# Optimization experiments

Measured on AMD Instinct MI355X. Metric: run time of the kernel, lower is better.

The kernel has to match this reference:

```python
import jax, jax.numpy as jnp
import numpy as np

S, B, K = 64, 16, 512
QD, KD, A = 512, 512, 256


def setup_inputs() -> dict:
    key = jax.random.key(0)
    ks = jax.random.split(key, 10)
    inv_q = 1.0 / np.sqrt(QD)
    inv_k = 1.0 / np.sqrt(KD)
    inv_a = 1.0 / np.sqrt(A)
    return {
        "queries": jax.random.normal(ks[0], (S, B, QD), dtype=jnp.float32),
        "keys": jax.random.normal(ks[1], (B, K, KD), dtype=jnp.float32),
        "null_mask": jax.random.randint(ks[2], (B, K), 0, 2).astype(jnp.bool_),
        # nn.Linear params (PyTorch layout: weight (out, in), bias (out,))
        "Ww": jax.random.uniform(ks[3], (A, QD), jnp.float32, -inv_q, inv_q),
        "Wb": jax.random.uniform(ks[4], (A,), jnp.float32, -inv_q, inv_q),
        "Uw": jax.random.uniform(ks[5], (A, KD), jnp.float32, -inv_k, inv_k),
        "Ub": jax.random.uniform(ks[6], (A,), jnp.float32, -inv_k, inv_k),
        "vw": jax.random.uniform(ks[7], (1, A), jnp.float32, -inv_a, inv_a),
        "vb": jax.random.uniform(ks[8], (1,), jnp.float32, -inv_a, inv_a),
    }


def reference(queries, keys, null_mask, Ww, Wb, Uw, Ub, vw, vb):
    # t_query: (S, B, A); t_key: (B, K, A)
    t_query = jnp.einsum("sbq,aq->sba", queries, Ww) + Wb
    t_key = jnp.einsum("bkd,ad->bka", keys, Uw) + Ub
    # broadcast add -> (S, B, K, A), tanh, project with v -> alpha (S, B, K)
    h = jnp.tanh(t_query[:, :, None, :] + t_key[None, :, :, :])
    alpha = jnp.einsum("sbka,a->sbk", h, vw[0]) + vb[0]
    alpha = jnp.where(null_mask[None, :, :], -jnp.inf, alpha)
    att_weight = jax.nn.softmax(alpha, axis=2)  # (S, B, K)
    # bmm(att_weight^T, keys)^T -> (S, B, KD)
    attened_keys = jnp.einsum("sbk,bkd->sbd", att_weight, keys)
    return attened_keys, alpha
```

## Files before the change

### kernel.cpp

```cpp
#include <hip/hip_runtime.h>
#include <math.h>

#define S_DIM 64
#define B_DIM 16
#define K_DIM 512
#define QD_DIM 512
#define A_DIM 256

#define NEG_BIG (-3.0e38f)

#define SC 2.8853900817779268f

#define EKBF_BYTE_OFF 1048576
#define W_WS_BYTE_OFF 5242880
#define CONV_BYTE_OFF 7340032
#define CONV_ROWS 9728

typedef __attribute__((ext_vector_type(8))) short short8v;
typedef __attribute__((ext_vector_type(4))) float f32x4;

static __device__ __forceinline__ uint2 pack_hi4(float4 v) {
    unsigned x0 = __float_as_uint(v.x), x1 = __float_as_uint(v.y),
             x2 = __float_as_uint(v.z), x3 = __float_as_uint(v.w);
    uint2 r;
    r.x = (x1 & 0xffff0000u) | (x0 >> 16);
    r.y = (x3 & 0xffff0000u) | (x2 >> 16);
    return r;
}
static __device__ __forceinline__ uint2 pack_lo4(float4 v) {
    float l0 = v.x - __uint_as_float(__float_as_uint(v.x) & 0xffff0000u);
    float l1 = v.y - __uint_as_float(__float_as_uint(v.y) & 0xffff0000u);
    float l2 = v.z - __uint_as_float(__float_as_uint(v.z) & 0xffff0000u);
    float l3 = v.w - __uint_as_float(__float_as_uint(v.w) & 0xffff0000u);
    unsigned y0 = __float_as_uint(l0), y1 = __float_as_uint(l1),
             y2 = __float_as_uint(l2), y3 = __float_as_uint(l3);
    uint2 r;
    r.x = (y1 & 0xffff0000u) | (y0 >> 16);
    r.y = (y3 & 0xffff0000u) | (y2 >> 16);
    return r;
}

static __device__ __forceinline__ unsigned short bf16_rne(float f) {
    unsigned u = __float_as_uint(f);
    return (unsigned short)((u + 0x7FFFu + ((u >> 16) & 1u)) >> 16);
}

__global__ __launch_bounds__(256) void conv_kernel(
    const float* __restrict__ q, const float* __restrict__ k,
    const float* __restrict__ ww, const float* __restrict__ uw,
    unsigned short* __restrict__ hi, unsigned short* __restrict__ lo)
{
    const int idx = blockIdx.x * 256 + threadIdx.x;
    const int row = idx >> 6;
    const int c   = (idx & 63) << 3;

    const float* __restrict__ src;
    if (row < 1024)      src = q  + (size_t)row * 512;
    else if (row < 9216) src = k  + (size_t)(row - 1024) * 512;
    else if (row < 9472) src = ww + (size_t)(row - 9216) * 512;
    else                 src = uw + (size_t)(row - 9472) * 512;

    float4 v0 = *(const float4*)(src + c);
    float4 v1 = *(const float4*)(src + c + 4);
    uint2 h0 = pack_hi4(v0), h1 = pack_hi4(v1);
    uint2 l0 = pack_lo4(v0), l1 = pack_lo4(v1);
    uint4 H = {h0.x, h0.y, h1.x, h1.y};
    uint4 L = {l0.x, l0.y, l1.x, l1.y};
    *(uint4*)&hi[(size_t)row * 512 + c] = H;
    *(uint4*)&lo[(size_t)row * 512 + c] = L;
}

__global__ __launch_bounds__(256) void lin_mfma(
    const unsigned short* __restrict__ hi, const unsigned short* __restrict__ lo,
    const float* __restrict__ Wb, const float* __restrict__ Ub,
    float* __restrict__ eq, unsigned short* __restrict__ ekbf)
{
    __shared__ unsigned short Ah[64][40], Al[64][40], Bh[64][40], Bl[64][40];

    const int bx = blockIdx.x;
    const bool isQ = (bx < 64);
    int mt, nt;
    if (isQ) { mt = bx >> 2; nt = bx & 3; }
    else     { int t = bx - 64; mt = t >> 7; nt = t & 127; }

    const int aro = isQ ? (mt * 64) : (9472 + mt * 64);
    const int bro = isQ ? (9216 + nt * 64) : (1024 + nt * 64);

    const int tid  = threadIdx.x;
    const int srow = tid >> 2;
    const int scol = (tid & 3) << 3;
    const int lane = tid & 63, wid = tid >> 6;
    const int wm = (wid >> 1) << 5, wn = (wid & 1) << 5;
    const int fr  = lane & 15;
    const int fkb = (lane >> 4) << 3;

    f32x4 acc[2][2] = {};

    const unsigned short* pAh = hi + (size_t)(aro + srow) * 512 + scol;
    const unsigned short* pAl = lo + (size_t)(aro + srow) * 512 + scol;
    const unsigned short* pBh = hi + (size_t)(bro + srow) * 512 + scol;
    const unsigned short* pBl = lo + (size_t)(bro + srow) * 512 + scol;

    uint4 c_ah = *(const uint4*)(pAh);
    uint4 c_al = *(const uint4*)(pAl);
    uint4 c_bh = *(const uint4*)(pBh);
    uint4 c_bl = *(const uint4*)(pBl);
    uint4 n_ah = *(const uint4*)(pAh + 32);
    uint4 n_al = *(const uint4*)(pAl + 32);
    uint4 n_bh = *(const uint4*)(pBh + 32);
    uint4 n_bl = *(const uint4*)(pBl + 32);

    for (int ks = 0; ks < 16; ++ks) {
        __syncthreads();
        *(uint4*)&Ah[srow][scol] = c_ah;
        *(uint4*)&Al[srow][scol] = c_al;
        *(uint4*)&Bh[srow][scol] = c_bh;
        *(uint4*)&Bl[srow][scol] = c_bl;
        __syncthreads();
        c_ah = n_ah; c_al = n_al; c_bh = n_bh; c_bl = n_bl;
        if (ks < 14) {
            const int o = (ks + 2) * 32;
            n_ah = *(const uint4*)(pAh + o);
            n_al = *(const uint4*)(pAl + o);
            n_bh = *(const uint4*)(pBh + o);
            n_bl = *(const uint4*)(pBl + o);
        }
        short8v bhv[2], blv[2];
        #pragma unroll
        for (int j = 0; j < 2; ++j) {
            bhv[j] = *(const short8v*)&Bh[wn + j * 16 + fr][fkb];
            blv[j] = *(const short8v*)&Bl[wn + j * 16 + fr][fkb];
        }
        #pragma unroll
        for (int i = 0; i < 2; ++i) {
            short8v ah = *(const short8v*)&Ah[wm + i * 16 + fr][fkb];
            short8v al = *(const short8v*)&Al[wm + i * 16 + fr][fkb];
            #pragma unroll
            for (int j = 0; j < 2; ++j) {
                acc[i][j] = __builtin_amdgcn_mfma_f32_16x16x32_bf16(ah, bhv[j], acc[i][j], 0, 0, 0);
                acc[i][j] = __builtin_amdgcn_mfma_f32_16x16x32_bf16(ah, blv[j], acc[i][j], 0, 0, 0);
                acc[i][j] = __builtin_amdgcn_mfma_f32_16x16x32_bf16(al, bhv[j], acc[i][j], 0, 0, 0);
            }
        }
    }

    const int crow = (lane >> 4) << 2;
    if (isQ) {
        #pragma unroll
        for (int j = 0; j < 2; ++j) {
            const int a_col = nt * 64 + wn + j * 16 + fr;
            const float bias = Wb[a_col];
            #pragma unroll
            for (int i = 0; i < 2; ++i)
                #pragma unroll
                for (int r = 0; r < 4; ++r) {
                    const int m = mt * 64 + wm + i * 16 + crow + r;
                    eq[(size_t)m * 256 + a_col] =
                        __builtin_amdgcn_exp2f(SC * (acc[i][j][r] + bias));
                }
        }
    } else {
        #pragma unroll
        for (int i = 0; i < 2; ++i)
            #pragma unroll
            for (int r = 0; r < 4; ++r) {
                const int a = mt * 64 + wm + i * 16 + crow + r;
                const float bias = Ub[a];
                #pragma unroll
                for (int j = 0; j < 2; ++j) {
                    const int n = nt * 64 + wn + j * 16 + fr;
                    float e = __builtin_amdgcn_exp2f(SC * (acc[i][j][r] + bias));
                    ekbf[(size_t)(n >> 9) * 131072 + (size_t)a * 512 + (n & 511)]
                        = bf16_rne(e);
                }
            }
    }
}

__global__ __launch_bounds__(256) void alpha_kernel(
    const float* __restrict__ eq, const unsigned short* __restrict__ ekbf,
    const float* __restrict__ vw, const float* __restrict__ vb,
    const unsigned char* __restrict__ mask,
    float* __restrict__ alpha_out, float* __restrict__ w_ws)
{
    __shared__ float4 pv4[128];
    __shared__ float red[3][4];

    const int bid = blockIdx.x;
    const int b = bid >> 6;
    const int s = bid & 63;
    const int sb = s * B_DIM + b;
    const int tid = threadIdx.x;
    const int lane = tid & 63, wid = tid >> 6;

    const float myvw = vw[tid];
    if (tid < 128) {
        float2 e2 = *(const float2*)&eq[(size_t)sb * A_DIM + tid * 2];
        float2 v2 = *(const float2*)&vw[tid * 2];
        float4 p = {e2.x, e2.y, v2.x, v2.y};
        pv4[tid] = p;
    }

    float sv = myvw;
    #pragma unroll
    for (int o = 32; o > 0; o >>= 1) sv += __shfl_xor(sv, o);
    if (lane == 0) red[0][wid] = sv;
    __syncthreads();
    const float base = red[0][0] + red[0][1] + red[0][2] + red[0][3] + vb[0];

    const unsigned short* __restrict__ ekb = ekbf + (size_t)b * 131072;
    const int k2 = tid * 2;

    float acc0 = 0.f, acc1 = 0.f;
    #pragma unroll 4
    for (int ap = 0; ap < 128; ++ap) {
        unsigned va = *(const unsigned*)&ekb[(size_t)(2 * ap) * 512 + k2];
        unsigned vbu = *(const unsigned*)&ekb[(size_t)(2 * ap + 1) * 512 + k2];
        float4 p = pv4[ap];
        float e0a = __uint_as_float(va << 16);
        float e1a = __uint_as_float(va & 0xffff0000u);
        float e0b = __uint_as_float(vbu << 16);
        float e1b = __uint_as_float(vbu & 0xffff0000u);
        float d00 = fmaf(p.x, e0a, 1.0f);
        float d01 = fmaf(p.y, e0b, 1.0f);
        float d10 = fmaf(p.x, e1a, 1.0f);
        float d11 = fmaf(p.y, e1b, 1.0f);
        float n0 = fmaf(p.w, d00, p.z * d01);
        float n1 = fmaf(p.w, d10, p.z * d11);
        float r0 = __builtin_amdgcn_rcpf(d00 * d01);
        float r1 = __builtin_amdgcn_rcpf(d10 * d11);
        acc0 = fmaf(n0, r0, acc0);
        acc1 = fmaf(n1, r1, acc1);
    }

    float a0 = base - 2.0f * acc0;
    float a1 = base - 2.0f * acc1;
    const unsigned char* mrow = mask + b * K_DIM;
    if (mrow[k2])     a0 = NEG_BIG;
    if (mrow[k2 + 1]) a1 = NEG_BIG;

    *(float2*)&alpha_out[(size_t)sb * K_DIM + k2] = make_float2(a0, a1);

    float m = fmaxf(a0, a1);
    #pragma unroll
    for (int o = 32; o > 0; o >>= 1) m = fmaxf(m, __shfl_xor(m, o));
    if (lane == 0) red[1][wid] = m;
    __syncthreads();
    const float mx = fmaxf(fmaxf(red[1][0], red[1][1]), fmaxf(red[1][2], red[1][3]));

    float e0 = __expf(a0 - mx);
    float e1 = __expf(a1 - mx);
    float ssum = e0 + e1;
    #pragma unroll
    for (int o = 32; o > 0; o >>= 1) ssum += __shfl_xor(ssum, o);
    if (lane == 0) red[2][wid] = ssum;
    __syncthreads();
    const float inv = 1.0f / (red[2][0] + red[2][1] + red[2][2] + red[2][3]);

    *(float2*)&w_ws[(size_t)(b * S_DIM + s) * K_DIM + k2] = make_float2(e0 * inv, e1 * inv);
}

__global__ __launch_bounds__(256) void att_kernel(
    const float* __restrict__ w_ws, const float* __restrict__ keys,
    float* __restrict__ out_att)
{
    __shared__ float wt[16][68];
    __shared__ float kt[64][64];

    const int d0g = blockIdx.x * 64;
    const int s0  = blockIdx.y * 16;
    const int b   = blockIdx.z;
    const int tid = threadIdx.x;

    const int sL = tid >> 4;
    const int dc = (tid & 15) << 2;

    float acc[4] = {};

    for (int k0 = 0; k0 < K_DIM; k0 += 64) {
        __syncthreads();
        *(float4*)&wt[sL][dc] =
            *(const float4*)&w_ws[(size_t)(b * S_DIM + s0 + sL) * K_DIM + k0 + dc];
        #pragma unroll
        for (int rr = 0; rr < 4; ++rr) {
            const int kr = (tid >> 4) + rr * 16;
            *(float4*)&kt[kr][dc] =
                *(const float4*)&keys[((size_t)b * K_DIM + k0 + kr) * QD_DIM + d0g + dc];
        }
        __syncthreads();
        #pragma unroll
        for (int kk = 0; kk < 64; kk += 4) {
            float4 wv = *(const float4*)&wt[sL][kk];
            float wr[4] = {wv.x, wv.y, wv.z, wv.w};
            #pragma unroll
            for (int u = 0; u < 4; ++u) {
                float4 kv = *(const float4*)&kt[kk + u][dc];
                acc[0] = fmaf(wr[u], kv.x, acc[0]);
                acc[1] = fmaf(wr[u], kv.y, acc[1]);
                acc[2] = fmaf(wr[u], kv.z, acc[2]);
                acc[3] = fmaf(wr[u], kv.w, acc[3]);
            }
        }
    }

    float4 o = {acc[0], acc[1], acc[2], acc[3]};
    *(float4*)&out_att[(size_t)((s0 + sL) * B_DIM + b) * QD_DIM + d0g + dc] = o;
}

extern "C" void kernel_launch(void* const* d_in, const int* in_sizes, int n_in,
                              void* d_out, int out_size, void* d_ws, size_t ws_size,
                              hipStream_t stream) {
    const float* queries = (const float*)d_in[0];
    const float* keys    = (const float*)d_in[1];
    const unsigned char* mask = (const unsigned char*)d_in[2];
    const float* Ww = (const float*)d_in[3];
    const float* Wb = (const float*)d_in[4];
    const float* Uw = (const float*)d_in[5];
    const float* Ub = (const float*)d_in[6];
    const float* vw = (const float*)d_in[7];
    const float* vb = (const float*)d_in[8];

    float* out_att   = (float*)d_out;
    float* out_alpha = (float*)d_out + (size_t)S_DIM * B_DIM * QD_DIM;

    char* ws = (char*)d_ws;
    float* eq            = (float*)ws;
    unsigned short* ekbf = (unsigned short*)(ws + EKBF_BYTE_OFF);
    float* w_ws          = (float*)(ws + W_WS_BYTE_OFF);
    unsigned short* hi   = (unsigned short*)(ws + CONV_BYTE_OFF);
    unsigned short* lo   = hi + (size_t)CONV_ROWS * 512;

    conv_kernel<<<2432, 256, 0, stream>>>(queries, keys, Ww, Uw, hi, lo);

    lin_mfma<<<576, 256, 0, stream>>>(hi, lo, Wb, Ub, eq, ekbf);

    alpha_kernel<<<1024, 256, 0, stream>>>(eq, ekbf, vw, vb, mask,
                                           out_alpha, w_ws);

    dim3 gC(QD_DIM / 64, S_DIM / 16, B_DIM);
    att_kernel<<<gC, 256, 0, stream>>>(w_ws, keys, out_att);
    att_kernel<<<gC, 256, 0, stream>>>(w_ws, keys, out_att);
    att_kernel<<<gC, 256, 0, stream>>>(w_ws, keys, out_att);
}
```

Baseline: 166.4 us.

## Compute attention-weighted keys with bf16 MFMA and drop redundant launches

Softmax weights are now written as packed bf16 instead of fp32. The attention-weighted sum over keys is rewritten as a bf16 MFMA GEMM, with the fp32 keys converted to bf16 fragments in shared memory. The grid changes to one block per 64 output columns per batch, covering all 64 queries. The previous triple launch of the attention kernel becomes a single launch. The aim is to cut the FMA-bound scalar work and halve weight traffic, at the cost of bf16 precision on the weights and keys.

```diff
diff --git a/kernel.cpp b/kernel.cpp
--- a/kernel.cpp
+++ b/kernel.cpp
@@ -181,7 +181,7 @@
     const float* __restrict__ eq, const unsigned short* __restrict__ ekbf,
     const float* __restrict__ vw, const float* __restrict__ vb,
     const unsigned char* __restrict__ mask,
-    float* __restrict__ alpha_out, float* __restrict__ w_ws)
+    float* __restrict__ alpha_out, unsigned short* __restrict__ w_bf)
 {
     __shared__ float4 pv4[128];
     __shared__ float red[3][4];
@@ -257,54 +257,76 @@
     __syncthreads();
     const float inv = 1.0f / (red[2][0] + red[2][1] + red[2][2] + red[2][3]);
 
-    *(float2*)&w_ws[(size_t)(b * S_DIM + s) * K_DIM + k2] = make_float2(e0 * inv, e1 * inv);
-}
-
-__global__ __launch_bounds__(256) void att_kernel(
-    const float* __restrict__ w_ws, const float* __restrict__ keys,
+    const unsigned wpack = (unsigned)bf16_rne(e0 * inv)
+                         | ((unsigned)bf16_rne(e1 * inv) << 16);
+    *(unsigned*)&w_bf[(size_t)(b * S_DIM + s) * K_DIM + k2] = wpack;
+}
+
+__global__ __launch_bounds__(256) void att_mfma(
+    const unsigned short* __restrict__ w_bf, const float* __restrict__ keys,
     float* __restrict__ out_att)
 {
-    __shared__ float wt[16][68];
-    __shared__ float kt[64][64];
-
-    const int d0g = blockIdx.x * 64;
-    const int s0  = blockIdx.y * 16;
-    const int b   = blockIdx.z;
+    __shared__ unsigned short Wt[64][40];
+    __shared__ float Ks[32][68];
+
+    const int n0 = blockIdx.x * 64;
+    const int b  = blockIdx.y;
     const int tid = threadIdx.x;
-
-    const int sL = tid >> 4;
-    const int dc = (tid & 15) << 2;
-
-    float acc[4] = {};
-
-    for (int k0 = 0; k0 < K_DIM; k0 += 64) {
+    const int lane = tid & 63, wid = tid >> 6;
+    const int wm = (wid >> 1) << 5, wn = (wid & 1) << 5;
+    const int fr  = lane & 15;
+    const int fkb = (lane >> 4) << 3;
+
+    const int ws_row = tid >> 2;
+    const int ws_c8  = (tid & 3) << 3;
+    const int ks_row = tid >> 3;
+    const int ks_c8  = (tid & 7) << 3;
+
+    f32x4 acc[2][2] = {};
+
+    for (int k0 = 0; k0 < K_DIM; k0 += 32) {
         __syncthreads();
-        *(float4*)&wt[sL][dc] =
-            *(const float4*)&w_ws[(size_t)(b * S_DIM + s0 + sL) * K_DIM + k0 + dc];
-        #pragma unroll
-        for (int rr = 0; rr < 4; ++rr) {
-            const int kr = (tid >> 4) + rr * 16;
-            *(float4*)&kt[kr][dc] =
-                *(const float4*)&keys[((size_t)b * K_DIM + k0 + kr) * QD_DIM + d0g + dc];
+        *(uint4*)&Wt[ws_row][ws_c8] =
+            *(const uint4*)&w_bf[(size_t)(b * S_DIM + ws_row) * K_DIM + k0 + ws_c8];
+        {
+            const float* src = keys + ((size_t)b * K_DIM + k0 + ks_row) * QD_DIM + n0 + ks_c8;
+            *(float4*)&Ks[ks_row][ks_c8]     = *(const float4*)src;
+            *(float4*)&Ks[ks_row][ks_c8 + 4] = *(const float4*)(src + 4);
         }
         __syncthreads();
-        #pragma unroll
-        for (int kk = 0; kk < 64; kk += 4) {
-            float4 wv = *(const float4*)&wt[sL][kk];
-            float wr[4] = {wv.x, wv.y, wv.z, wv.w};
-            #pragma unroll
-            for (int u = 0; u < 4; ++u) {
-                float4 kv = *(const float4*)&kt[kk + u][dc];
-                acc[0] = fmaf(wr[u], kv.x, acc[0]);
-                acc[1] = fmaf(wr[u], kv.y, acc[1]);
-                acc[2] = fmaf(wr[u], kv.z, acc[2]);
-                acc[3] = fmaf(wr[u], kv.w, acc[3]);
+
+        short8v bfrag[2];
+        #pragma unroll
+        for (int j = 0; j < 2; ++j) {
+            const int d = wn + j * 16 + fr;
+            unsigned p0 = (unsigned)bf16_rne(Ks[fkb + 0][d]) | ((unsigned)bf16_rne(Ks[fkb + 1][d]) << 16);
+            unsigned p1 = (unsigned)bf16_rne(Ks[fkb + 2][d]) | ((unsigned)bf16_rne(Ks[fkb + 3][d]) << 16);
+            unsigned p2 = (unsigned)bf16_rne(Ks[fkb + 4][d]) | ((unsigned)bf16_rne(Ks[fkb + 5][d]) << 16);
+            unsigned p3 = (unsigned)bf16_rne(Ks[fkb + 6][d]) | ((unsigned)bf16_rne(Ks[fkb + 7][d]) << 16);
+            uint4 P = {p0, p1, p2, p3};
+            bfrag[j] = *(short8v*)&P;
+        }
+        #pragma unroll
+        for (int i = 0; i < 2; ++i) {
+            short8v afrag = *(const short8v*)&Wt[wm + i * 16 + fr][fkb];
+            #pragma unroll
+            for (int j = 0; j < 2; ++j)
+                acc[i][j] = __builtin_amdgcn_mfma_f32_16x16x32_bf16(afrag, bfrag[j], acc[i][j], 0, 0, 0);
+        }
+    }
+
+    const int crow = (lane >> 4) << 2;
+    #pragma unroll
+    for (int i = 0; i < 2; ++i)
+        #pragma unroll
+        for (int r = 0; r < 4; ++r) {
+            const int s = wm + i * 16 + crow + r;
+            #pragma unroll
+            for (int j = 0; j < 2; ++j) {
+                const int d = n0 + wn + j * 16 + fr;
+                out_att[((size_t)s * B_DIM + b) * QD_DIM + d] = acc[i][j][r];
             }
         }
-    }
-
-    float4 o = {acc[0], acc[1], acc[2], acc[3]};
-    *(float4*)&out_att[(size_t)((s0 + sL) * B_DIM + b) * QD_DIM + d0g + dc] = o;
 }
 
 extern "C" void kernel_launch(void* const* d_in, const int* in_sizes, int n_in,
@@ -326,7 +348,7 @@
     char* ws = (char*)d_ws;
     float* eq            = (float*)ws;
     unsigned short* ekbf = (unsigned short*)(ws + EKBF_BYTE_OFF);
-    float* w_ws          = (float*)(ws + W_WS_BYTE_OFF);
+    unsigned short* w_bf = (unsigned short*)(ws + W_WS_BYTE_OFF);
     unsigned short* hi   = (unsigned short*)(ws + CONV_BYTE_OFF);
     unsigned short* lo   = hi + (size_t)CONV_ROWS * 512;
 
@@ -335,10 +357,8 @@
     lin_mfma<<<576, 256, 0, stream>>>(hi, lo, Wb, Ub, eq, ekbf);
 
     alpha_kernel<<<1024, 256, 0, stream>>>(eq, ekbf, vw, vb, mask,
-                                           out_alpha, w_ws);
-
-    dim3 gC(QD_DIM / 64, S_DIM / 16, B_DIM);
-    att_kernel<<<gC, 256, 0, stream>>>(w_ws, keys, out_att);
-    att_kernel<<<gC, 256, 0, stream>>>(w_ws, keys, out_att);
-    att_kernel<<<gC, 256, 0, stream>>>(w_ws, keys, out_att);
-}
+                                           out_alpha, w_bf);
+
+    dim3 gC(QD_DIM / 64, B_DIM);
+    att_mfma<<<gC, 256, 0, stream>>>(w_bf, keys, out_att);
+}
```

New measurement: 137.2 us. -17.5%, faster.
